# Optimization experiments

Hardware: AMD Instinct MI355X
Metric: run time of the kernel (lower is better)

The kernel has to match this reference:

```python
import jax, jax.numpy as jnp
import numpy as np

B = 2048          # batch of latent vectors
NW = 32           # n_windows = floor(4096 / 128)
D = 128           # split_size == window_size == codebook dim
K = 2048          # codebook entries


def setup_inputs() -> dict:
    key = jax.random.key(0)
    k1, k2 = jax.random.split(key)
    ze = jax.random.normal(k1, (B, NW * D), dtype=jnp.float32)
    codebook = jax.random.normal(k2, (K, D), dtype=jnp.float32)
    return {"ze": ze, "codebook": codebook}


def reference(ze, codebook):
    # Window-based VQ: original loops over NW windows of width D along the
    # last axis; contiguous equal-width slices == reshape, so vectorize.
    Kc, Dc = codebook.shape
    zw = ze.reshape(ze.shape[0], -1, Dc)                      # [B, NW, D]
    # squared distances: ||z||^2 + ||c||^2 - 2 z.c  -> [B, NW, K]
    sq = (jnp.sum(zw * zw, axis=-1, keepdims=True)
          + jnp.sum(codebook * codebook, axis=1)
          - 2.0 * jnp.einsum('bwd,kd->bwk', zw, codebook))
    idx = jnp.argmin(sq, axis=-1)                             # [B, NW]
    zq = jnp.take(codebook, idx, axis=0)                      # [B, NW, D]
    return zq.reshape(ze.shape)
```

## Files before the change

kernel.cpp:

```cpp
#include <hip/hip_runtime.h>
#include <hip/hip_bf16.h>


#define VQ_D 128
#define VQ_K 2048
#define VQ_M 65536
#define VQ_THR 0.04f

typedef short short8 __attribute__((ext_vector_type(8)));
typedef int  int4v  __attribute__((ext_vector_type(4)));
typedef int  i32x16 __attribute__((ext_vector_type(16)));
typedef unsigned long long u64;

__device__ uint4 g_cbi[VQ_K * 16];
__device__ int   g_list[VQ_M];
__device__ u64   g_res[VQ_M];
__device__ int   g_count;

__global__ void vq_prepn(const float* __restrict__ cb, float2* __restrict__ cs2) {
    int g = blockIdx.x * 256 + threadIdx.x;
    int r = g >> 4, t = g & 15;
    const float4* s = reinterpret_cast<const float4*>(cb) + (size_t)g * 2;
    float4 f0 = s[0], f1 = s[1];
    float z[8] = {f0.x, f0.y, f0.z, f0.w, f1.x, f1.y, f1.z, f1.w};
    float ss = ((z[0]*z[0] + z[1]*z[1]) + (z[2]*z[2] + z[3]*z[3]))
             + ((z[4]*z[4] + z[5]*z[5]) + (z[6]*z[6] + z[7]*z[7]));
    float ax = fmaxf(fmaxf(fmaxf(fabsf(z[0]), fabsf(z[1])), fmaxf(fabsf(z[2]), fabsf(z[3]))),
                     fmaxf(fmaxf(fabsf(z[4]), fabsf(z[5])), fmaxf(fabsf(z[6]), fabsf(z[7]))));
    ss += __shfl_xor(ss, 1); ax = fmaxf(ax, __shfl_xor(ax, 1));
    ss += __shfl_xor(ss, 2); ax = fmaxf(ax, __shfl_xor(ax, 2));
    ss += __shfl_xor(ss, 4); ax = fmaxf(ax, __shfl_xor(ax, 4));
    ss += __shfl_xor(ss, 8); ax = fmaxf(ax, __shfl_xor(ax, 8));
    float mx  = fmaxf(ax, 1e-20f);
    float s1  = mx * (1.0f / 127.0f);
    float inv = 127.0f / mx;
    float inv2 = inv * 256.0f;
    int qa[8], qr[8];
    #pragma unroll
    for (int i = 0; i < 8; ++i) {
        float qf = rintf(z[i] * inv);
        float r1 = fmaf(-qf, s1, z[i]);
        float q2f = fminf(127.f, fmaxf(-127.f, rintf(r1 * inv2)));
        qa[i] = (int)qf; qr[i] = (int)q2f;
    }
    uint2 w1, w2;
    w1.x = (qa[0]&255) | ((qa[1]&255)<<8) | ((qa[2]&255)<<16) | ((unsigned)(qa[3]&255)<<24);
    w1.y = (qa[4]&255) | ((qa[5]&255)<<8) | ((qa[6]&255)<<16) | ((unsigned)(qa[7]&255)<<24);
    w2.x = (qr[0]&255) | ((qr[1]&255)<<8) | ((qr[2]&255)<<16) | ((unsigned)(qr[3]&255)<<24);
    w2.y = (qr[4]&255) | ((qr[5]&255)<<8) | ((qr[6]&255)<<16) | ((unsigned)(qr[7]&255)<<24);
    uint2* cw = reinterpret_cast<uint2*>(g_cbi);
    int c1 = (t >> 1) ^ (r & 15);
    int c2 = (8 + (t >> 1)) ^ (r & 15);
    cw[(r * 16 + c1) * 2 + (t & 1)] = w1;
    cw[(r * 16 + c2) * 2 + (t & 1)] = w2;
    if (t == 0) cs2[r] = make_float2(ss, s1);
    if (g == 0) g_count = 0;
}

__global__ __launch_bounds__(256, 2)
void vq_score(const float* __restrict__ ze,
              const float2* __restrict__ cs2,
              int* __restrict__ outIdx) {
    __shared__ uint4 sB[2048];
    const int tid  = threadIdx.x;
    const int lane = tid & 63;
    const int wv   = tid >> 6;
    const int ln31 = lane & 31;
    const int g2   = lane >> 5;
    const int qb   = blockIdx.x * 128;

    uint2 q1w[8], q2w[8];
    float s1r[8];
    #pragma unroll
    for (int jj = 0; jj < 8; ++jj) {
        int id = wv * 512 + jj * 64 + lane, r = id >> 4, t = id & 15;
        const float4* src =
            reinterpret_cast<const float4*>(ze + (size_t)(qb + r) * VQ_D + t * 8);
        float4 f0 = src[0], f1 = src[1];
        float z[8] = {f0.x, f0.y, f0.z, f0.w, f1.x, f1.y, f1.z, f1.w};
        float ax = fmaxf(fmaxf(fmaxf(fabsf(z[0]), fabsf(z[1])), fmaxf(fabsf(z[2]), fabsf(z[3]))),
                         fmaxf(fmaxf(fabsf(z[4]), fabsf(z[5])), fmaxf(fabsf(z[6]), fabsf(z[7]))));
        ax = fmaxf(ax, __shfl_xor(ax, 1));
        ax = fmaxf(ax, __shfl_xor(ax, 2));
        ax = fmaxf(ax, __shfl_xor(ax, 4));
        ax = fmaxf(ax, __shfl_xor(ax, 8));
        float mx  = fmaxf(ax, 1e-20f);
        float s1  = mx * (1.0f / 127.0f);
        float inv = 127.0f / mx;
        float inv2 = inv * 256.0f;
        s1r[jj] = s1;
        int qa[8], qr[8];
        #pragma unroll
        for (int i = 0; i < 8; ++i) {
            float qf = rintf(z[i] * inv);
            float r1 = fmaf(-qf, s1, z[i]);
            float q2f = fminf(127.f, fmaxf(-127.f, rintf(r1 * inv2)));
            qa[i] = (int)qf; qr[i] = (int)q2f;
        }
        q1w[jj].x = (qa[0]&255) | ((qa[1]&255)<<8) | ((qa[2]&255)<<16) | ((unsigned)(qa[3]&255)<<24);
        q1w[jj].y = (qa[4]&255) | ((qa[5]&255)<<8) | ((qa[6]&255)<<16) | ((unsigned)(qa[7]&255)<<24);
        q2w[jj].x = (qr[0]&255) | ((qr[1]&255)<<8) | ((qr[2]&255)<<16) | ((unsigned)(qr[3]&255)<<24);
        q2w[jj].y = (qr[4]&255) | ((qr[5]&255)<<8) | ((qr[6]&255)<<16) | ((unsigned)(qr[7]&255)<<24);
    }
    {
        uint2* sw = reinterpret_cast<uint2*>(sB);
        #pragma unroll
        for (int jj = 0; jj < 8; ++jj) {
            int id = wv * 512 + jj * 64 + lane, r = id >> 4, t = id & 15;
            int c1 = (t >> 1) ^ (r & 15);
            int c2 = (8 + (t >> 1)) ^ (r & 15);
            sw[(r * 16 + c1) * 2 + (t & 1)] = q1w[jj];
            sw[(r * 16 + c2) * 2 + (t & 1)] = q2w[jj];
        }
    }
    float mj[16];
    #pragma unroll
    for (int j = 0; j < 16; ++j) {
        float va = __shfl(s1r[2 * (j >> 2)],     (j & 3) << 4);
        float vb = __shfl(s1r[2 * (j >> 2) + 1], (j & 3) << 4);
        mj[j] = (g2 ? vb : va) * (-1.0f / 128.0f);
    }
    __syncthreads();
    int4v aq1[4], aq2[4];
    {
        int r = wv * 32 + ln31;
        #pragma unroll
        for (int kc = 0; kc < 4; ++kc) {
            int c = kc * 2 + g2;
            aq1[kc] = *(const int4v*)&sB[r * 16 + (c ^ (r & 15))];
            aq2[kc] = *(const int4v*)&sB[r * 16 + ((8 + c) ^ (r & 15))];
        }
    }
    __syncthreads();

    #define STAGE_B(T, BUF)                                                     \
        _Pragma("unroll")                                                       \
        for (int jj = 0; jj < 4; ++jj) {                                        \
            int base = wv * 256 + jj * 64;                                      \
            __builtin_amdgcn_global_load_lds(                                   \
                (const void*)(g_cbi + (size_t)(T) * 1024 + base + lane),        \
                (void*)(sB + (BUF) * 1024 + base), 16, 0, 0);                   \
        }
    STAGE_B(0, 0)

    float m1[16], m2[16];
    int   i1[16];
    #pragma unroll
    for (int j = 0; j < 16; ++j) { m1[j] = 3.0e38f; m2[j] = 3.0e38f; i1[j] = 0; }

    i32x16 Z;
    #pragma unroll
    for (int j = 0; j < 16; ++j) Z[j] = 0;

    float2 cf0 = cs2[ln31];
    float2 cf1 = cs2[32 + ln31];
    const int x15 = ln31 & 15;

    for (int tile = 0; tile < VQ_K / 64; ++tile) {
        asm volatile("s_waitcnt vmcnt(0)" ::: "memory");
        __builtin_amdgcn_s_barrier();
        __builtin_amdgcn_sched_barrier(0);

        const int bb = (tile & 1) << 10;

        if (tile < VQ_K / 64 - 1) { STAGE_B(tile + 1, (tile + 1) & 1) }
        int nt = (tile + 1) & (VQ_K / 64 - 1);
        float2 nf0 = cs2[nt * 64 + ln31];
        float2 nf1 = cs2[nt * 64 + 32 + ln31];

        int kb = tile * 64 + ln31;

        {
            i32x16 HH, XX;
            __builtin_amdgcn_s_setprio(1);
            {
                int c  = g2;
                int p1 = c ^ x15, p2 = (8 + c) ^ x15;
                int4v bh = *(const int4v*)&sB[bb + ln31 * 16 + p1];
                int4v bl = *(const int4v*)&sB[bb + ln31 * 16 + p2];
                XX = __builtin_amdgcn_mfma_i32_32x32x32_i8(aq2[0], bh, Z, 0, 0, 0);
                HH = __builtin_amdgcn_mfma_i32_32x32x32_i8(aq1[0], bh, Z, 0, 0, 0);
                XX = __builtin_amdgcn_mfma_i32_32x32x32_i8(aq1[0], bl, XX, 0, 0, 0);
            }
            #pragma unroll
            for (int kc = 1; kc < 4; ++kc) {
                int c  = kc * 2 + g2;
                int p1 = c ^ x15, p2 = (8 + c) ^ x15;
                int4v bh = *(const int4v*)&sB[bb + ln31 * 16 + p1];
                int4v bl = *(const int4v*)&sB[bb + ln31 * 16 + p2];
                XX = __builtin_amdgcn_mfma_i32_32x32x32_i8(aq2[kc], bh, XX, 0, 0, 0);
                HH = __builtin_amdgcn_mfma_i32_32x32x32_i8(aq1[kc], bh, HH, 0, 0, 0);
                XX = __builtin_amdgcn_mfma_i32_32x32x32_i8(aq1[kc], bl, XX, 0, 0, 0);
            }
            __builtin_amdgcn_s_setprio(0);

            #pragma unroll
            for (int j = 0; j < 16; ++j) {
                float s0 = fmaf((float)((HH[j] << 8) + XX[j]) * cf0.y, mj[j], cf0.x);
                bool lt0 = s0 < m1[j];
                m2[j] = __builtin_amdgcn_fmed3f(s0, m1[j], m2[j]);
                i1[j] = lt0 ? kb : i1[j];
                m1[j] = fminf(m1[j], s0);
            }
        }

        {
            i32x16 HH, XX;
            __builtin_amdgcn_s_setprio(1);
            {
                int c  = g2;
                int p1 = c ^ x15, p2 = (8 + c) ^ x15;
                int4v bh = *(const int4v*)&sB[bb + (32 + ln31) * 16 + p1];
                int4v bl = *(const int4v*)&sB[bb + (32 + ln31) * 16 + p2];
                XX = __builtin_amdgcn_mfma_i32_32x32x32_i8(aq2[0], bh, Z, 0, 0, 0);
                HH = __builtin_amdgcn_mfma_i32_32x32x32_i8(aq1[0], bh, Z, 0, 0, 0);
                XX = __builtin_amdgcn_mfma_i32_32x32x32_i8(aq1[0], bl, XX, 0, 0, 0);
            }
            #pragma unroll
            for (int kc = 1; kc < 4; ++kc) {
                int c  = kc * 2 + g2;
                int p1 = c ^ x15, p2 = (8 + c) ^ x15;
                int4v bh = *(const int4v*)&sB[bb + (32 + ln31) * 16 + p1];
                int4v bl = *(const int4v*)&sB[bb + (32 + ln31) * 16 + p2];
                XX = __builtin_amdgcn_mfma_i32_32x32x32_i8(aq2[kc], bh, XX, 0, 0, 0);
                HH = __builtin_amdgcn_mfma_i32_32x32x32_i8(aq1[kc], bh, HH, 0, 0, 0);
                XX = __builtin_amdgcn_mfma_i32_32x32x32_i8(aq1[kc], bl, XX, 0, 0, 0);
            }
            __builtin_amdgcn_s_setprio(0);

            #pragma unroll
            for (int j = 0; j < 16; ++j) {
                float s1v = fmaf((float)((HH[j] << 8) + XX[j]) * cf1.y, mj[j], cf1.x);
                bool lt1 = s1v < m1[j];
                m2[j] = __builtin_amdgcn_fmed3f(s1v, m1[j], m2[j]);
                i1[j] = lt1 ? kb + 32 : i1[j];
                m1[j] = fminf(m1[j], s1v);
            }
        }

        cf0 = nf0; cf1 = nf1;
    }

    #pragma unroll
    for (int j = 0; j < 16; ++j) {
        float a1v = m1[j], a2v = m2[j];
        int   ai  = i1[j];
        #pragma unroll
        for (int off = 1; off < 32; off <<= 1) {
            float o1 = __shfl_xor(a1v, off);
            float o2 = __shfl_xor(a2v, off);
            int   oi = __shfl_xor(ai, off);
            bool lt = o1 < a1v;
            float hi = lt ? a1v : o1;
            a1v = lt ? o1 : a1v;
            ai  = lt ? oi : ai;
            a2v = fminf(fminf(a2v, o2), hi);
        }
        if (ln31 == 0) {
            int row = qb + wv * 32 + (j & 3) + 8 * (j >> 2) + 4 * g2;
            if (a2v - a1v < VQ_THR) {
                outIdx[row] = (int)((unsigned)ai | 0x80000000u);
                g_res[row] = ~0ull;
                int pos = atomicAdd(&g_count, 1);
                g_list[pos] = row;
            } else {
                outIdx[row] = ai;
            }
        }
    }
    #undef STAGE_B
}

__global__ __launch_bounds__(256)
void vq_rescue(const float* __restrict__ ze,
               const float* __restrict__ cb,
               const float2* __restrict__ cs2) {
    __shared__ float cs[64 * 132];
    __shared__ float zs[4][128];

    const int tid  = threadIdx.x;
    const int lane = tid & 63;
    const int wv   = tid >> 6;
    const int count = g_count;
    const long nitems = (long)((count + 3) >> 2) * 32;

    for (long it = blockIdx.x; it < nitems; it += gridDim.x) {
        const int grp   = (int)(it >> 5);
        const int chunk = (int)(it & 31);
        const int slot  = grp * 4 + wv;
        const bool valid = slot < count;
        const int row = g_list[valid ? slot : (count - 1)];

        #pragma unroll
        for (int j = 0; j < 8; ++j) {
            int id = j * 256 + tid;
            int r = id >> 5, col = id & 31;
            float4 v = reinterpret_cast<const float4*>(cb)[(size_t)(chunk * 64 + r) * 32 + col];
            *reinterpret_cast<float4*>(&cs[r * 132 + col * 4]) = v;
        }
        if (tid < 128) {
            int w = tid >> 5, i = tid & 31;
            int s2 = grp * 4 + w; if (s2 >= count) s2 = count - 1;
            int rw = g_list[s2];
            float4 v = reinterpret_cast<const float4*>(ze)[(size_t)rw * 32 + i];
            *reinterpret_cast<float4*>(&zs[w][i * 4]) = v;
        }
        __syncthreads();

        if (valid) {
            float4 zn = {0.f, 0.f, 0.f, 0.f};
            #pragma unroll
            for (int i = 0; i < 32; ++i) {
                float4 z = *reinterpret_cast<const float4*>(&zs[wv][i * 4]);
                zn.x += z.x * z.x; zn.y += z.y * z.y;
                zn.z += z.z * z.z; zn.w += z.w * z.w;
            }
            float znorm = (zn.x + zn.y) + (zn.z + zn.w);

            int k = chunk * 64 + lane;
            float4 a = {0.f, 0.f, 0.f, 0.f};
            #pragma unroll
            for (int i = 0; i < 32; ++i) {
                float4 c = *reinterpret_cast<const float4*>(&cs[lane * 132 + i * 4]);
                float4 z = *reinterpret_cast<const float4*>(&zs[wv][i * 4]);
                a.x += z.x * c.x; a.y += z.y * c.y;
                a.z += z.z * c.z; a.w += z.w * c.w;
            }
            float dot = (a.x + a.y) + (a.z + a.w);
            float s = fmaf(-2.f, dot, znorm + cs2[k].x);

            u64 p = ((u64)__float_as_uint(s) << 32) | (unsigned)k;
            #pragma unroll
            for (int o = 1; o < 64; o <<= 1) {
                u64 q = __shfl_xor(p, o);
                p = q < p ? q : p;
            }
            if (lane == 0) atomicMin(&g_res[row], p);
        }
        __syncthreads();
    }
}

__global__ void vq_gather(const float* __restrict__ cb,
                          const int* __restrict__ idx,
                          float* __restrict__ out) {
    size_t u = (size_t)blockIdx.x * blockDim.x + threadIdx.x;
    int r = (int)(u >> 5);
    int j = (int)(u & 31);
    int v = idx[r];
    if (v < 0) v = (int)(g_res[r] & 0xFFFFFFFFull);
    reinterpret_cast<float4*>(out)[u] =
        reinterpret_cast<const float4*>(cb)[((size_t)v << 5) + j];
}

extern "C" void kernel_launch(void* const* d_in, const int* in_sizes, int n_in,
                              void* d_out, int out_size, void* d_ws, size_t ws_size,
                              hipStream_t stream) {
    const float* ze = (const float*)d_in[0];
    const float* cb = (const float*)d_in[1];
    float* out = (float*)d_out;

    float2* cs2  = (float2*)d_ws;
    int*    bidx = (int*)((char*)d_ws + 16384);

    vq_prepn<<<VQ_K * VQ_D / 8 / 256, 256, 0, stream>>>(cb, cs2);
    vq_score<<<VQ_M / 128, 256, 0, stream>>>(ze, cs2, bidx);
    vq_rescue<<<1024, 256, 0, stream>>>(ze, cb, cs2);
    vq_gather<<<(VQ_M * (VQ_D / 4)) / 256, 256, 0, stream>>>(cb, bidx, out);
}
```

Before: 112.6 us.

## Split codebook scan across two block halves and merge partial argmins

The scoring kernel now launches twice as many blocks, each scanning half of the codebook (1024 entries) for a 128-row query tile, and writes per-row partial top-2 distances and indices to global buffers. A new merge kernel combines the two halves, applies the near-tie threshold, and queues ambiguous rows for exact rescue. Launch bounds are raised to request 4 blocks per CU, and the rescue threshold is halved to send fewer rows to the fp32 rescue pass. The split costs an extra kernel launch, redundant query quantisation in both halves, and extra global traffic for the partial results. The tighter threshold risks wrong indices where the int8 approximation error exceeds it.

```diff
diff --git a/kernel.cpp b/kernel.cpp
--- a/kernel.cpp
+++ b/kernel.cpp
@@ -5,17 +5,19 @@
 #define VQ_D 128
 #define VQ_K 2048
 #define VQ_M 65536
-#define VQ_THR 0.04f
+#define VQ_THR 0.02f
 
 typedef short short8 __attribute__((ext_vector_type(8)));
 typedef int  int4v  __attribute__((ext_vector_type(4)));
 typedef int  i32x16 __attribute__((ext_vector_type(16)));
 typedef unsigned long long u64;
 
-__device__ uint4 g_cbi[VQ_K * 16];
-__device__ int   g_list[VQ_M];
-__device__ u64   g_res[VQ_M];
-__device__ int   g_count;
+__device__ uint4  g_cbi[VQ_K * 16];
+__device__ int    g_list[VQ_M];
+__device__ u64    g_res[VQ_M];
+__device__ int    g_count;
+__device__ float2 g_pm[2][VQ_M];
+__device__ int    g_pi[2][VQ_M];
 
 __global__ void vq_prepn(const float* __restrict__ cb, float2* __restrict__ cs2) {
     int g = blockIdx.x * 256 + threadIdx.x;
@@ -57,17 +59,19 @@
     if (g == 0) g_count = 0;
 }
 
-__global__ __launch_bounds__(256, 2)
+__global__ __launch_bounds__(256, 4)
 void vq_score(const float* __restrict__ ze,
-              const float2* __restrict__ cs2,
-              int* __restrict__ outIdx) {
+              const float2* __restrict__ cs2) {
     __shared__ uint4 sB[2048];
     const int tid  = threadIdx.x;
     const int lane = tid & 63;
     const int wv   = tid >> 6;
     const int ln31 = lane & 31;
     const int g2   = lane >> 5;
-    const int qb   = blockIdx.x * 128;
+    const int half = blockIdx.x >> 9;
+    const int qb   = (blockIdx.x & 511) * 128;
+    const int kofs = half << 10;
+    const int kt0  = half << 4;
 
     uint2 q1w[8], q2w[8];
     float s1r[8];
@@ -138,7 +142,7 @@
         for (int jj = 0; jj < 4; ++jj) {                                        \
             int base = wv * 256 + jj * 64;                                      \
             __builtin_amdgcn_global_load_lds(                                   \
-                (const void*)(g_cbi + (size_t)(T) * 1024 + base + lane),        \
+                (const void*)(g_cbi + (size_t)(kt0 + (T)) * 1024 + base + lane),\
                 (void*)(sB + (BUF) * 1024 + base), 16, 0, 0);                   \
         }
     STAGE_B(0, 0)
@@ -152,23 +156,23 @@
     #pragma unroll
     for (int j = 0; j < 16; ++j) Z[j] = 0;
 
-    float2 cf0 = cs2[ln31];
-    float2 cf1 = cs2[32 + ln31];
+    float2 cf0 = cs2[kofs + ln31];
+    float2 cf1 = cs2[kofs + 32 + ln31];
     const int x15 = ln31 & 15;
 
-    for (int tile = 0; tile < VQ_K / 64; ++tile) {
+    for (int tile = 0; tile < 16; ++tile) {
         asm volatile("s_waitcnt vmcnt(0)" ::: "memory");
         __builtin_amdgcn_s_barrier();
         __builtin_amdgcn_sched_barrier(0);
 
         const int bb = (tile & 1) << 10;
 
-        if (tile < VQ_K / 64 - 1) { STAGE_B(tile + 1, (tile + 1) & 1) }
-        int nt = (tile + 1) & (VQ_K / 64 - 1);
-        float2 nf0 = cs2[nt * 64 + ln31];
-        float2 nf1 = cs2[nt * 64 + 32 + ln31];
-
-        int kb = tile * 64 + ln31;
+        if (tile < 15) { STAGE_B(tile + 1, (tile + 1) & 1) }
+        int nt = (tile + 1) & 15;
+        float2 nf0 = cs2[kofs + nt * 64 + ln31];
+        float2 nf1 = cs2[kofs + nt * 64 + 32 + ln31];
+
+        int kb = kofs + tile * 64 + ln31;
 
         {
             i32x16 HH, XX;
@@ -258,17 +262,30 @@
         }
         if (ln31 == 0) {
             int row = qb + wv * 32 + (j & 3) + 8 * (j >> 2) + 4 * g2;
-            if (a2v - a1v < VQ_THR) {
-                outIdx[row] = (int)((unsigned)ai | 0x80000000u);
-                g_res[row] = ~0ull;
-                int pos = atomicAdd(&g_count, 1);
-                g_list[pos] = row;
-            } else {
-                outIdx[row] = ai;
-            }
+            g_pm[half][row] = make_float2(a1v, a2v);
+            g_pi[half][row] = ai;
         }
     }
     #undef STAGE_B
+}
+
+__global__ void vq_merge(int* __restrict__ outIdx) {
+    int row = blockIdx.x * 256 + threadIdx.x;
+    float2 a = g_pm[0][row]; int ia = g_pi[0][row];
+    float2 b = g_pm[1][row]; int ib = g_pi[1][row];
+    bool af = a.x <= b.x;
+    float w1 = af ? a.x : b.x;
+    int   wi = af ? ia  : ib;
+    float hi = af ? b.x : a.x;
+    float w2 = fminf(fminf(a.y, b.y), hi);
+    if (w2 - w1 < VQ_THR) {
+        outIdx[row] = (int)((unsigned)wi | 0x80000000u);
+        g_res[row] = ~0ull;
+        int pos = atomicAdd(&g_count, 1);
+        g_list[pos] = row;
+    } else {
+        outIdx[row] = wi;
+    }
 }
 
 __global__ __launch_bounds__(256)
@@ -364,7 +381,8 @@
     int*    bidx = (int*)((char*)d_ws + 16384);
 
     vq_prepn<<<VQ_K * VQ_D / 8 / 256, 256, 0, stream>>>(cb, cs2);
-    vq_score<<<VQ_M / 128, 256, 0, stream>>>(ze, cs2, bidx);
+    vq_score<<<VQ_M / 128 * 2, 256, 0, stream>>>(ze, cs2);
+    vq_merge<<<VQ_M / 256, 256, 0, stream>>>(bidx);
     vq_rescue<<<1024, 256, 0, stream>>>(ze, cb, cs2);
     vq_gather<<<(VQ_M * (VQ_D / 4)) / 256, 256, 0, stream>>>(cb, bidx, out);
 }
```

Measured after the change: 417.0 us. +270.4%, slower.

## Load codebook tiles directly from global memory and tighten rescue threshold

Applied to the files above, without the earlier changes.

The main scan loop no longer stages int8 codebook tiles into double-buffered LDS with global_load_lds and per-tile barriers. Each lane now reads its swizzled B fragments straight from the global (L2/cache-resident) codebook buffer, advancing a pointer per tile. This removes the barrier and waitcnt stalls of the LDS pipeline, but every wave re-reads the codebook through the cache hierarchy and its memory latency sits right before the MFMAs. The ambiguity threshold is also halved, so fewer rows are flagged for the exact fp32 rescue pass, at some risk to correctness margin.

```diff
diff --git a/kernel.cpp b/kernel.cpp
--- a/kernel.cpp
+++ b/kernel.cpp
@@ -5,7 +5,7 @@
 #define VQ_D 128
 #define VQ_K 2048
 #define VQ_M 65536
-#define VQ_THR 0.04f
+#define VQ_THR 0.02f
 
 typedef short short8 __attribute__((ext_vector_type(8)));
 typedef int  int4v  __attribute__((ext_vector_type(4)));
@@ -131,17 +131,16 @@
             aq2[kc] = *(const int4v*)&sB[r * 16 + ((8 + c) ^ (r & 15))];
         }
     }
-    __syncthreads();
-
-    #define STAGE_B(T, BUF)                                                     \
-        _Pragma("unroll")                                                       \
-        for (int jj = 0; jj < 4; ++jj) {                                        \
-            int base = wv * 256 + jj * 64;                                      \
-            __builtin_amdgcn_global_load_lds(                                   \
-                (const void*)(g_cbi + (size_t)(T) * 1024 + base + lane),        \
-                (void*)(sB + (BUF) * 1024 + base), 16, 0, 0);                   \
-        }
-    STAGE_B(0, 0)
+
+    const int x15 = ln31 & 15;
+    unsigned oh[4], ol[4];
+    #pragma unroll
+    for (int kc = 0; kc < 4; ++kc) {
+        int c = kc * 2 + g2;
+        oh[kc] = (unsigned)((ln31 * 16 + (c ^ x15)) * 16);
+        ol[kc] = (unsigned)((ln31 * 16 + ((8 + c) ^ x15)) * 16);
+    }
+    const char* cb8 = (const char*)g_cbi;
 
     float m1[16], m2[16];
     int   i1[16];
@@ -154,16 +153,8 @@
 
     float2 cf0 = cs2[ln31];
     float2 cf1 = cs2[32 + ln31];
-    const int x15 = ln31 & 15;
 
     for (int tile = 0; tile < VQ_K / 64; ++tile) {
-        asm volatile("s_waitcnt vmcnt(0)" ::: "memory");
-        __builtin_amdgcn_s_barrier();
-        __builtin_amdgcn_sched_barrier(0);
-
-        const int bb = (tile & 1) << 10;
-
-        if (tile < VQ_K / 64 - 1) { STAGE_B(tile + 1, (tile + 1) & 1) }
         int nt = (tile + 1) & (VQ_K / 64 - 1);
         float2 nf0 = cs2[nt * 64 + ln31];
         float2 nf1 = cs2[nt * 64 + 32 + ln31];
@@ -174,20 +165,16 @@
             i32x16 HH, XX;
             __builtin_amdgcn_s_setprio(1);
             {
-                int c  = g2;
-                int p1 = c ^ x15, p2 = (8 + c) ^ x15;
-                int4v bh = *(const int4v*)&sB[bb + ln31 * 16 + p1];
-                int4v bl = *(const int4v*)&sB[bb + ln31 * 16 + p2];
+                int4v bh = *(const int4v*)(cb8 + oh[0]);
+                int4v bl = *(const int4v*)(cb8 + ol[0]);
                 XX = __builtin_amdgcn_mfma_i32_32x32x32_i8(aq2[0], bh, Z, 0, 0, 0);
                 HH = __builtin_amdgcn_mfma_i32_32x32x32_i8(aq1[0], bh, Z, 0, 0, 0);
                 XX = __builtin_amdgcn_mfma_i32_32x32x32_i8(aq1[0], bl, XX, 0, 0, 0);
             }
             #pragma unroll
             for (int kc = 1; kc < 4; ++kc) {
-                int c  = kc * 2 + g2;
-                int p1 = c ^ x15, p2 = (8 + c) ^ x15;
-                int4v bh = *(const int4v*)&sB[bb + ln31 * 16 + p1];
-                int4v bl = *(const int4v*)&sB[bb + ln31 * 16 + p2];
+                int4v bh = *(const int4v*)(cb8 + oh[kc]);
+                int4v bl = *(const int4v*)(cb8 + ol[kc]);
                 XX = __builtin_amdgcn_mfma_i32_32x32x32_i8(aq2[kc], bh, XX, 0, 0, 0);
                 HH = __builtin_amdgcn_mfma_i32_32x32x32_i8(aq1[kc], bh, HH, 0, 0, 0);
                 XX = __builtin_amdgcn_mfma_i32_32x32x32_i8(aq1[kc], bl, XX, 0, 0, 0);
@@ -208,20 +195,16 @@
             i32x16 HH, XX;
             __builtin_amdgcn_s_setprio(1);
             {
-                int c  = g2;
-                int p1 = c ^ x15, p2 = (8 + c) ^ x15;
-                int4v bh = *(const int4v*)&sB[bb + (32 + ln31) * 16 + p1];
-                int4v bl = *(const int4v*)&sB[bb + (32 + ln31) * 16 + p2];
+                int4v bh = *(const int4v*)(cb8 + (oh[0] + 8192u));
+                int4v bl = *(const int4v*)(cb8 + (ol[0] + 8192u));
                 XX = __builtin_amdgcn_mfma_i32_32x32x32_i8(aq2[0], bh, Z, 0, 0, 0);
                 HH = __builtin_amdgcn_mfma_i32_32x32x32_i8(aq1[0], bh, Z, 0, 0, 0);
                 XX = __builtin_amdgcn_mfma_i32_32x32x32_i8(aq1[0], bl, XX, 0, 0, 0);
             }
             #pragma unroll
             for (int kc = 1; kc < 4; ++kc) {
-                int c  = kc * 2 + g2;
-                int p1 = c ^ x15, p2 = (8 + c) ^ x15;
-                int4v bh = *(const int4v*)&sB[bb + (32 + ln31) * 16 + p1];
-                int4v bl = *(const int4v*)&sB[bb + (32 + ln31) * 16 + p2];
+                int4v bh = *(const int4v*)(cb8 + (oh[kc] + 8192u));
+                int4v bl = *(const int4v*)(cb8 + (ol[kc] + 8192u));
                 XX = __builtin_amdgcn_mfma_i32_32x32x32_i8(aq2[kc], bh, XX, 0, 0, 0);
                 HH = __builtin_amdgcn_mfma_i32_32x32x32_i8(aq1[kc], bh, HH, 0, 0, 0);
                 XX = __builtin_amdgcn_mfma_i32_32x32x32_i8(aq1[kc], bl, XX, 0, 0, 0);
@@ -238,6 +221,7 @@
             }
         }
 
+        cb8 += 16384;
         cf0 = nf0; cf1 = nf1;
     }
 
@@ -268,7 +252,6 @@
             }
         }
     }
-    #undef STAGE_B
 }
 
 __global__ __launch_bounds__(256)
```

After: 113.3 us. About the same (+0.6%).
